# Kernel optimization log

Hardware: AMD Instinct MI355X
Metric: run time of the kernel (lower is better)

The kernel has to match this reference:

```python
import jax, jax.numpy as jnp
import numpy as np

NUM_HEADS = 14
NUM_KV_HEADS = 2
HEAD_DIM = 64
HIDDEN = 896
ROPE_THETA = 1000000.0
NEG_INF = -1e9


def _rope_tables(seq_len, dtype=jnp.float32):
    inv_freq = 1.0 / (ROPE_THETA ** (jnp.arange(0, HEAD_DIM, 2, dtype=jnp.float32) / HEAD_DIM))
    t = jnp.arange(seq_len, dtype=jnp.float32)
    freqs = t[:, None] * inv_freq[None, :]          # [S, hd/2]
    emb = jnp.concatenate((freqs, freqs), axis=-1)  # [S, hd]
    return jnp.cos(emb).astype(dtype), jnp.sin(emb).astype(dtype)


def _rotate_half(x):
    x1, x2 = x[..., : x.shape[-1] // 2], x[..., x.shape[-1] // 2 :]
    return jnp.concatenate((-x2, x1), axis=-1)


def setup_inputs() -> dict:
    key = jax.random.key(0)
    ks = jax.random.split(key, 6)
    B, S = 2, 2048
    hidden_states = jax.random.normal(ks[0], (B, S, HIDDEN), dtype=jnp.float32)
    # additive causal mask [1, 1, S, S]
    causal = jnp.tril(jnp.ones((S, S), dtype=bool))
    attention_mask = jnp.where(causal, 0.0, NEG_INF).astype(jnp.float32)[None, None]
    sd = 1.0 / np.sqrt(HIDDEN)
    Wq = jax.random.normal(ks[1], (HIDDEN, NUM_HEADS * HEAD_DIM), dtype=jnp.float32) * sd
    bq = jnp.zeros((NUM_HEADS * HEAD_DIM,), dtype=jnp.float32)
    Wk = jax.random.normal(ks[2], (HIDDEN, NUM_KV_HEADS * HEAD_DIM), dtype=jnp.float32) * sd
    bk = jnp.zeros((NUM_KV_HEADS * HEAD_DIM,), dtype=jnp.float32)
    Wv = jax.random.normal(ks[3], (HIDDEN, NUM_KV_HEADS * HEAD_DIM), dtype=jnp.float32) * sd
    bv = jnp.zeros((NUM_KV_HEADS * HEAD_DIM,), dtype=jnp.float32)
    Wo = jax.random.normal(ks[4], (NUM_HEADS * HEAD_DIM, HIDDEN), dtype=jnp.float32) * sd
    return {
        'hidden_states': hidden_states, 'attention_mask': attention_mask,
        'Wq': Wq, 'bq': bq, 'Wk': Wk, 'bk': bk, 'Wv': Wv, 'bv': bv, 'Wo': Wo,
    }


def reference(hidden_states, attention_mask, Wq, bq, Wk, bk, Wv, bv, Wo):
    B, S, _ = hidden_states.shape
    n_groups = NUM_HEADS // NUM_KV_HEADS
    q = (hidden_states @ Wq + bq).reshape(B, S, NUM_HEADS, HEAD_DIM)
    k = (hidden_states @ Wk + bk).reshape(B, S, NUM_KV_HEADS, HEAD_DIM)
    v = (hidden_states @ Wv + bv).reshape(B, S, NUM_KV_HEADS, HEAD_DIM)

    cos, sin = _rope_tables(S, hidden_states.dtype)
    cos = cos[None, :, None, :]
    sin = sin[None, :, None, :]
    q = q * cos + _rotate_half(q) * sin
    k = k * cos + _rotate_half(k) * sin

    # GQA: repeat kv heads to match query heads
    k = jnp.repeat(k, n_groups, axis=2)  # [B, S, nH, hd]
    v = jnp.repeat(v, n_groups, axis=2)

    q = q.transpose(0, 2, 1, 3)  # [B, nH, S, hd]
    k = k.transpose(0, 2, 1, 3)
    v = v.transpose(0, 2, 1, 3)

    scores = jnp.einsum('bhqd,bhkd->bhqk', q, k) / jnp.sqrt(jnp.float32(HEAD_DIM)).astype(q.dtype)
    scores = scores + attention_mask
    attn = jax.nn.softmax(scores, axis=-1)
    out = jnp.einsum('bhqk,bhkd->bhqd', attn, v)        # [B, nH, S, hd]
    out = out.transpose(0, 2, 1, 3).reshape(B, S, -1)   # [B, S, nH*hd]
    return out @ Wo
```

## Files before the change

### kernel.cpp

```cpp
#include <hip/hip_runtime.h>
#include <hip/hip_bf16.h>
#include <math.h>

#define NH 14
#define NKV 2
#define HD 64
#define HID 896
#define SEQ 2048
#define BATCH 2

typedef __attribute__((ext_vector_type(8))) short short8;
typedef __attribute__((ext_vector_type(4))) float f32x4;
typedef unsigned short ushort_t;

__device__ __forceinline__ unsigned short f2b(float f) {
    unsigned int u = __float_as_uint(f);
    unsigned int r = (u + 0x7fffu + ((u >> 16) & 1u)) >> 16;
    return (unsigned short)r;
}

__global__ __launch_bounds__(256) void xcast_kernel(
    const float* __restrict__ X, ushort_t* __restrict__ Xb)
{
    size_t i = ((size_t)blockIdx.x * 256 + threadIdx.x) * 8;
    float4 a = *(const float4*)(X + i);
    float4 b = *(const float4*)(X + i + 4);
    short8 o;
    o[0] = f2b(a.x); o[1] = f2b(a.y); o[2] = f2b(a.z); o[3] = f2b(a.w);
    o[4] = f2b(b.x); o[5] = f2b(b.y); o[6] = f2b(b.z); o[7] = f2b(b.w);
    *(short8*)(Xb + i) = o;
}

__global__ __launch_bounds__(256) void wtrans_kernel(
    const float* __restrict__ Wq, const float* __restrict__ Wk,
    const float* __restrict__ Wv, const float* __restrict__ Wo,
    ushort_t* __restrict__ WqkvT, ushort_t* __restrict__ WoT)
{
    __shared__ float tile[32][33];
    const int tx = threadIdx.x, ty = threadIdx.y;
    const int z = blockIdx.z;
    const float* src; ushort_t* dst; int N, rowoff;
    if      (z == 0) { src = Wq; dst = WqkvT; N = HID; rowoff = 0;    }
    else if (z == 1) { src = Wk; dst = WqkvT; N = 128; rowoff = 896;  }
    else if (z == 2) { src = Wv; dst = WqkvT; N = 128; rowoff = 1024; }
    else             { src = Wo; dst = WoT;   N = HID; rowoff = 0;    }
    const int k0 = blockIdx.x * 32;
    const int n0 = blockIdx.y * 32;
    if (n0 >= N) return;
    #pragma unroll
    for (int i = 0; i < 4; ++i)
        tile[ty * 4 + i][tx] = src[(size_t)(k0 + ty * 4 + i) * N + n0 + tx];
    __syncthreads();
    #pragma unroll
    for (int i = 0; i < 4; ++i)
        dst[(size_t)(rowoff + n0 + ty * 4 + i) * HID + k0 + tx]
            = f2b(tile[tx][ty * 4 + i]);
}

#define LDA 40
__global__ __launch_bounds__(256) void qkv_kernel(
    const ushort_t* __restrict__ Xb, const ushort_t* __restrict__ WqkvT,
    const float* __restrict__ bq, const float* __restrict__ bk,
    const float* __restrict__ bv,
    ushort_t* __restrict__ qbuf, ushort_t* __restrict__ kbuf,
    ushort_t* __restrict__ vbuf)
{
    __shared__ ushort_t Asb[128 * LDA];
    __shared__ ushort_t Bsb[64 * LDA];
    const int tid  = threadIdx.x;
    const int w    = tid >> 6;
    const int lane = tid & 63;
    const int quad = lane >> 4;
    const int l16  = lane & 15;
    const int m0 = blockIdx.x * 128;
    const int nt = blockIdx.y;
    const int nb = nt * 64;

    f32x4 acc[2][4];
    #pragma unroll
    for (int mf = 0; mf < 2; ++mf)
        #pragma unroll
        for (int nf = 0; nf < 4; ++nf) acc[mf][nf] = (f32x4){0.f, 0.f, 0.f, 0.f};

    for (int k0 = 0; k0 < HID; k0 += 32) {
        #pragma unroll
        for (int j = 0; j < 2; ++j) {
            int u = tid + j * 256;
            int row = u >> 2, c8 = u & 3;
            *(short8*)&Asb[row * LDA + c8 * 8] =
                *(const short8*)(Xb + (size_t)(m0 + row) * HID + k0 + c8 * 8);
        }
        {
            int row = tid >> 2, c8 = tid & 3;
            *(short8*)&Bsb[row * LDA + c8 * 8] =
                *(const short8*)(WqkvT + (size_t)(nb + row) * HID + k0 + c8 * 8);
        }
        __syncthreads();
        const ushort_t* Ab = &Asb[(w * 32 + l16) * LDA + quad * 8];
        short8 a0 = *(const short8*)Ab;
        short8 a1 = *(const short8*)(Ab + 16 * LDA);
        #pragma unroll
        for (int nf = 0; nf < 4; ++nf) {
            short8 bf = *(const short8*)&Bsb[(nf * 16 + l16) * LDA + quad * 8];
            acc[0][nf] = __builtin_amdgcn_mfma_f32_16x16x32_bf16(a0, bf, acc[0][nf], 0, 0, 0);
            acc[1][nf] = __builtin_amdgcn_mfma_f32_16x16x32_bf16(a1, bf, acc[1][nf], 0, 0, 0);
        }
        __syncthreads();
    }

    float bcol[4];
    #pragma unroll
    for (int f = 0; f < 4; ++f) {
        int d = f * 16 + l16;
        bcol[f] = (nt < 14) ? bq[nt * 64 + d]
                : (nt < 16) ? bk[(nt - 14) * 64 + d]
                            : bv[(nt - 16) * 64 + d];
    }
    const float lnth = 13.815510558f;
    float if0 = expf(-((float)l16)        / 32.0f * lnth);
    float if1 = expf(-((float)(l16 + 16)) / 32.0f * lnth);

    #pragma unroll
    for (int mf = 0; mf < 2; ++mf)
        #pragma unroll
        for (int r = 0; r < 4; ++r) {
            int grow = m0 + w * 32 + mf * 16 + quad * 4 + r;
            int b = grow >> 11;
            int s = grow & 2047;
            float v0 = acc[mf][0][r] + bcol[0];
            float v1 = acc[mf][1][r] + bcol[1];
            float v2 = acc[mf][2][r] + bcol[2];
            float v3 = acc[mf][3][r] + bcol[3];
            if (nt < 16) {
                float s0, c0, s1, c1;
                sincosf((float)s * if0, &s0, &c0);
                sincosf((float)s * if1, &s1, &c1);
                float n0 = v0 * c0 - v2 * s0;
                float n2 = v2 * c0 + v0 * s0;
                float n1 = v1 * c1 - v3 * s1;
                float n3 = v3 * c1 + v1 * s1;
                v0 = n0; v1 = n1; v2 = n2; v3 = n3;
            }
            if (nt < 14) {
                ushort_t* dst = qbuf + ((size_t)(b * NH + nt) * SEQ + s) * HD;
                dst[l16]      = f2b(v0);
                dst[l16 + 16] = f2b(v1);
                dst[l16 + 32] = f2b(v2);
                dst[l16 + 48] = f2b(v3);
            } else if (nt < 16) {
                ushort_t* dst = kbuf + ((size_t)(b * NKV + nt - 14) * SEQ + s) * HD;
                dst[l16]      = f2b(v0);
                dst[l16 + 16] = f2b(v1);
                dst[l16 + 32] = f2b(v2);
                dst[l16 + 48] = f2b(v3);
            } else {
                ushort_t* dst = vbuf + (size_t)(b * NKV + nt - 16) * HD * SEQ + s;
                dst[(size_t)(l16)      * SEQ] = f2b(v0);
                dst[(size_t)(l16 + 16) * SEQ] = f2b(v1);
                dst[(size_t)(l16 + 32) * SEQ] = f2b(v2);
                dst[(size_t)(l16 + 48) * SEQ] = f2b(v3);
            }
        }
}

#define LDP 72
__global__ __launch_bounds__(256) void attn_kernel(
    const ushort_t* __restrict__ qbuf, const ushort_t* __restrict__ kbuf,
    const ushort_t* __restrict__ vbuf, ushort_t* __restrict__ abuf)
{
    __shared__ ushort_t Ks[64 * LDP];
    __shared__ ushort_t Vt[64 * LDP];
    __shared__ ushort_t Ps[4][16 * LDP];

    const int tid  = threadIdx.x;
    const int w    = tid >> 6;
    const int lane = tid & 63;
    const int quad = lane >> 4;
    const int l16  = lane & 15;
    const int bi = blockIdx.x;
    const int h  = blockIdx.y;
    const int b  = blockIdx.z;
    const int kvh = h / (NH / NKV);

    const ushort_t* kb_h = kbuf + (size_t)(b * NKV + kvh) * SEQ * HD;
    const ushort_t* vt_h = vbuf + (size_t)(b * NKV + kvh) * HD * SEQ;

    for (int pass = 0; pass < 2; ++pass) {
        const int qt = pass ? (31 - bi) : bi;

        const ushort_t* qrow =
            qbuf + ((size_t)((b * NH + h) * SEQ) + qt * 64 + w * 16 + l16) * HD;
        short8 qf0 = *(const short8*)(qrow + quad * 8);
        short8 qf1 = *(const short8*)(qrow + 32 + quad * 8);

        f32x4 O[4];
        float m_i[4], l_i[4];
        #pragma unroll
        for (int n = 0; n < 4; ++n) O[n] = (f32x4){0.f, 0.f, 0.f, 0.f};
        #pragma unroll
        for (int r = 0; r < 4; ++r) { m_i[r] = -1e30f; l_i[r] = 0.0f; }

        for (int kt = 0; kt <= qt; ++kt) {
            __syncthreads();
            for (int i = tid; i < 512; i += 256) {
                int row = i >> 3, c8 = i & 7;
                *(short8*)&Ks[row * LDP + c8 * 8] =
                    *(const short8*)(kb_h + ((size_t)(kt * 64 + row)) * HD + c8 * 8);
                *(short8*)&Vt[row * LDP + c8 * 8] =
                    *(const short8*)(vt_h + (size_t)row * SEQ + kt * 64 + c8 * 8);
            }
            __syncthreads();

            f32x4 S[4];
            #pragma unroll
            for (int f = 0; f < 4; ++f) {
                S[f] = (f32x4){0.f, 0.f, 0.f, 0.f};
                short8 kf0 = *(const short8*)&Ks[(f * 16 + l16) * LDP + quad * 8];
                short8 kf1 = *(const short8*)&Ks[(f * 16 + l16) * LDP + 32 + quad * 8];
                S[f] = __builtin_amdgcn_mfma_f32_16x16x32_bf16(qf0, kf0, S[f], 0, 0, 0);
                S[f] = __builtin_amdgcn_mfma_f32_16x16x32_bf16(qf1, kf1, S[f], 0, 0, 0);
            }

            const bool diag = (kt == qt);
            float sc[4][4];
            #pragma unroll
            for (int f = 0; f < 4; ++f)
                #pragma unroll
                for (int r = 0; r < 4; ++r) {
                    float v = S[f][r] * 0.125f;
                    if (diag && (f * 16 + l16) > (w * 16 + quad * 4 + r)) v = -1e30f;
                    sc[f][r] = v;
                }

            float pm[4];
            #pragma unroll
            for (int r = 0; r < 4; ++r)
                pm[r] = fmaxf(fmaxf(sc[0][r], sc[1][r]), fmaxf(sc[2][r], sc[3][r]));
            #pragma unroll
            for (int off = 1; off < 16; off <<= 1)
                #pragma unroll
                for (int r = 0; r < 4; ++r)
                    pm[r] = fmaxf(pm[r], __shfl_xor(pm[r], off));

            float alpha[4], psum[4];
            #pragma unroll
            for (int r = 0; r < 4; ++r) {
                float mnew = fmaxf(m_i[r], pm[r]);
                alpha[r] = __expf(m_i[r] - mnew);
                m_i[r] = mnew;
                psum[r] = 0.0f;
            }
            #pragma unroll
            for (int f = 0; f < 4; ++f)
                #pragma unroll
                for (int r = 0; r < 4; ++r) {
                    float p = __expf(sc[f][r] - m_i[r]);
                    sc[f][r] = p;
                    psum[r] += p;
                }
            #pragma unroll
            for (int off = 1; off < 16; off <<= 1)
                #pragma unroll
                for (int r = 0; r < 4; ++r)
                    psum[r] += __shfl_xor(psum[r], off);
            #pragma unroll
            for (int r = 0; r < 4; ++r)
                l_i[r] = l_i[r] * alpha[r] + psum[r];
            #pragma unroll
            for (int n = 0; n < 4; ++n)
                #pragma unroll
                for (int r = 0; r < 4; ++r)
                    O[n][r] *= alpha[r];

            #pragma unroll
            for (int f = 0; f < 4; ++f)
                #pragma unroll
                for (int r = 0; r < 4; ++r)
                    Ps[w][(quad * 4 + r) * LDP + f * 16 + l16] = f2b(sc[f][r]);
            short8 pa0 = *(const short8*)&Ps[w][l16 * LDP + quad * 8];
            short8 pa1 = *(const short8*)&Ps[w][l16 * LDP + 32 + quad * 8];

            #pragma unroll
            for (int n = 0; n < 4; ++n) {
                short8 vf0 = *(const short8*)&Vt[(n * 16 + l16) * LDP + quad * 8];
                short8 vf1 = *(const short8*)&Vt[(n * 16 + l16) * LDP + 32 + quad * 8];
                O[n] = __builtin_amdgcn_mfma_f32_16x16x32_bf16(pa0, vf0, O[n], 0, 0, 0);
                O[n] = __builtin_amdgcn_mfma_f32_16x16x32_bf16(pa1, vf1, O[n], 0, 0, 0);
            }
        }

        float inv[4];
        #pragma unroll
        for (int r = 0; r < 4; ++r) inv[r] = 1.0f / l_i[r];
        #pragma unroll
        for (int n = 0; n < 4; ++n)
            #pragma unroll
            for (int r = 0; r < 4; ++r) {
                int rowg = qt * 64 + w * 16 + quad * 4 + r;
                abuf[(size_t)(b * SEQ + rowg) * HID + h * HD + n * 16 + l16]
                    = f2b(O[n][r] * inv[r]);
            }
    }
}

__global__ __launch_bounds__(256) void oproj_kernel(
    const ushort_t* __restrict__ A, const ushort_t* __restrict__ WoT,
    float* __restrict__ out)
{
    __shared__ ushort_t Asb[128 * LDA];
    __shared__ ushort_t Bsb[64 * LDA];
    const int tid  = threadIdx.x;
    const int w    = tid >> 6;
    const int lane = tid & 63;
    const int quad = lane >> 4;
    const int l16  = lane & 15;
    const int m0 = blockIdx.x * 128;
    const int n0 = blockIdx.y * 64;

    f32x4 acc[2][4];
    #pragma unroll
    for (int mf = 0; mf < 2; ++mf)
        #pragma unroll
        for (int nf = 0; nf < 4; ++nf) acc[mf][nf] = (f32x4){0.f, 0.f, 0.f, 0.f};

    for (int k0 = 0; k0 < HID; k0 += 32) {
        #pragma unroll
        for (int j = 0; j < 2; ++j) {
            int u = tid + j * 256;
            int row = u >> 2, c8 = u & 3;
            *(short8*)&Asb[row * LDA + c8 * 8] =
                *(const short8*)(A + (size_t)(m0 + row) * HID + k0 + c8 * 8);
        }
        {
            int row = tid >> 2, c8 = tid & 3;
            *(short8*)&Bsb[row * LDA + c8 * 8] =
                *(const short8*)(WoT + (size_t)(n0 + row) * HID + k0 + c8 * 8);
        }
        __syncthreads();
        const ushort_t* Ab = &Asb[(w * 32 + l16) * LDA + quad * 8];
        short8 a0 = *(const short8*)Ab;
        short8 a1 = *(const short8*)(Ab + 16 * LDA);
        #pragma unroll
        for (int nf = 0; nf < 4; ++nf) {
            short8 bf = *(const short8*)&Bsb[(nf * 16 + l16) * LDA + quad * 8];
            acc[0][nf] = __builtin_amdgcn_mfma_f32_16x16x32_bf16(a0, bf, acc[0][nf], 0, 0, 0);
            acc[1][nf] = __builtin_amdgcn_mfma_f32_16x16x32_bf16(a1, bf, acc[1][nf], 0, 0, 0);
        }
        __syncthreads();
    }

    #pragma unroll
    for (int mf = 0; mf < 2; ++mf)
        #pragma unroll
        for (int r = 0; r < 4; ++r) {
            size_t rbase = (size_t)(m0 + w * 32 + mf * 16 + quad * 4 + r) * HID + n0;
            #pragma unroll
            for (int f = 0; f < 4; ++f)
                out[rbase + f * 16 + l16] = acc[mf][f][r];
        }
}

extern "C" void kernel_launch(void* const* d_in, const int* in_sizes, int n_in,
                              void* d_out, int out_size, void* d_ws, size_t ws_size,
                              hipStream_t stream) {
    const float* X  = (const float*)d_in[0];
    const float* Wq = (const float*)d_in[2];
    const float* bq = (const float*)d_in[3];
    const float* Wk = (const float*)d_in[4];
    const float* bk = (const float*)d_in[5];
    const float* Wv = (const float*)d_in[6];
    const float* bv = (const float*)d_in[7];
    const float* Wo = (const float*)d_in[8];
    float* out = (float*)d_out;

    ushort_t* ws    = (ushort_t*)d_ws;
    ushort_t* Xb    = ws;
    ushort_t* WqkvT = Xb    + 3670016;
    ushort_t* WoT   = WqkvT + 1032192;
    ushort_t* qbuf  = WoT   + 802816;
    ushort_t* kbuf  = qbuf  + 3670016;
    ushort_t* vbuf  = kbuf  + 524288;
    ushort_t* abufb = vbuf  + 524288;

    xcast_kernel<<<dim3(1792), 256, 0, stream>>>(X, Xb);
    wtrans_kernel<<<dim3(28, 28, 4), dim3(32, 8), 0, stream>>>(
        Wq, Wk, Wv, Wo, WqkvT, WoT);
    qkv_kernel<<<dim3(32, 18), 256, 0, stream>>>(
        Xb, WqkvT, bq, bk, bv, qbuf, kbuf, vbuf);
    attn_kernel<<<dim3(16, NH, BATCH), 256, 0, stream>>>(
        qbuf, kbuf, vbuf, abufb);
    oproj_kernel<<<dim3(32, 14), 256, 0, stream>>>(
        abufb, WoT, out);
}
```

Baseline: 212.9 us.

## Restructure attention with transposed S, register-resident P, fp16 V and diagonal skipping

The attention kernel now computes S transposed (K as the A operand), so each lane owns one query row. This makes the softmax reductions two shuffles instead of four, and P can feed a 16x16x16 fp16 MFMA directly from registers, removing the shared-memory P round trip. V is stored as fp16, the 1/sqrt(d) scale is folded into Q in the projection kernel, and MFMAs on fully masked diagonal sub-tiles are skipped. The grid now launches one q-tile per block, longest first, instead of pairing tiles, which adds more blocks but risks load imbalance. The P and V products now run in fp16 instead of bf16.

```diff
diff --git a/kernel.cpp b/kernel.cpp
--- a/kernel.cpp
+++ b/kernel.cpp
@@ -10,7 +10,9 @@
 #define BATCH 2
 
 typedef __attribute__((ext_vector_type(8))) short short8;
+typedef __attribute__((ext_vector_type(4))) short short4v;
 typedef __attribute__((ext_vector_type(4))) float f32x4;
+typedef __attribute__((ext_vector_type(4))) _Float16 half4;
 typedef unsigned short ushort_t;
 
 __device__ __forceinline__ unsigned short f2b(float f) {
@@ -63,7 +65,7 @@
     const float* __restrict__ bq, const float* __restrict__ bk,
     const float* __restrict__ bv,
     ushort_t* __restrict__ qbuf, ushort_t* __restrict__ kbuf,
-    ushort_t* __restrict__ vbuf)
+    _Float16* __restrict__ vbuf)
 {
     __shared__ ushort_t Asb[128 * LDA];
     __shared__ ushort_t Bsb[64 * LDA];
@@ -143,10 +145,10 @@
             }
             if (nt < 14) {
                 ushort_t* dst = qbuf + ((size_t)(b * NH + nt) * SEQ + s) * HD;
-                dst[l16]      = f2b(v0);
-                dst[l16 + 16] = f2b(v1);
-                dst[l16 + 32] = f2b(v2);
-                dst[l16 + 48] = f2b(v3);
+                dst[l16]      = f2b(v0 * 0.125f);
+                dst[l16 + 16] = f2b(v1 * 0.125f);
+                dst[l16 + 32] = f2b(v2 * 0.125f);
+                dst[l16 + 48] = f2b(v3 * 0.125f);
             } else if (nt < 16) {
                 ushort_t* dst = kbuf + ((size_t)(b * NKV + nt - 14) * SEQ + s) * HD;
                 dst[l16]      = f2b(v0);
@@ -154,11 +156,11 @@
                 dst[l16 + 32] = f2b(v2);
                 dst[l16 + 48] = f2b(v3);
             } else {
-                ushort_t* dst = vbuf + (size_t)(b * NKV + nt - 16) * HD * SEQ + s;
-                dst[(size_t)(l16)      * SEQ] = f2b(v0);
-                dst[(size_t)(l16 + 16) * SEQ] = f2b(v1);
-                dst[(size_t)(l16 + 32) * SEQ] = f2b(v2);
-                dst[(size_t)(l16 + 48) * SEQ] = f2b(v3);
+                _Float16* dst = vbuf + (size_t)(b * NKV + nt - 16) * HD * SEQ + s;
+                dst[(size_t)(l16)      * SEQ] = (_Float16)v0;
+                dst[(size_t)(l16 + 16) * SEQ] = (_Float16)v1;
+                dst[(size_t)(l16 + 32) * SEQ] = (_Float16)v2;
+                dst[(size_t)(l16 + 48) * SEQ] = (_Float16)v3;
             }
         }
 }
@@ -166,140 +168,125 @@
 #define LDP 72
 __global__ __launch_bounds__(256) void attn_kernel(
     const ushort_t* __restrict__ qbuf, const ushort_t* __restrict__ kbuf,
-    const ushort_t* __restrict__ vbuf, ushort_t* __restrict__ abuf)
+    const _Float16* __restrict__ vbuf, ushort_t* __restrict__ abuf)
 {
     __shared__ ushort_t Ks[64 * LDP];
-    __shared__ ushort_t Vt[64 * LDP];
-    __shared__ ushort_t Ps[4][16 * LDP];
+    __shared__ _Float16 Vt[64 * LDP];
 
     const int tid  = threadIdx.x;
     const int w    = tid >> 6;
     const int lane = tid & 63;
     const int quad = lane >> 4;
     const int l16  = lane & 15;
-    const int bi = blockIdx.x;
+    const int qt = 31 - blockIdx.x;
     const int h  = blockIdx.y;
     const int b  = blockIdx.z;
     const int kvh = h / (NH / NKV);
+    const int myrow = w * 16 + l16;
 
     const ushort_t* kb_h = kbuf + (size_t)(b * NKV + kvh) * SEQ * HD;
-    const ushort_t* vt_h = vbuf + (size_t)(b * NKV + kvh) * HD * SEQ;
-
-    for (int pass = 0; pass < 2; ++pass) {
-        const int qt = pass ? (31 - bi) : bi;
-
-        const ushort_t* qrow =
-            qbuf + ((size_t)((b * NH + h) * SEQ) + qt * 64 + w * 16 + l16) * HD;
-        short8 qf0 = *(const short8*)(qrow + quad * 8);
-        short8 qf1 = *(const short8*)(qrow + 32 + quad * 8);
-
-        f32x4 O[4];
-        float m_i[4], l_i[4];
-        #pragma unroll
-        for (int n = 0; n < 4; ++n) O[n] = (f32x4){0.f, 0.f, 0.f, 0.f};
-        #pragma unroll
-        for (int r = 0; r < 4; ++r) { m_i[r] = -1e30f; l_i[r] = 0.0f; }
-
-        for (int kt = 0; kt <= qt; ++kt) {
-            __syncthreads();
-            for (int i = tid; i < 512; i += 256) {
-                int row = i >> 3, c8 = i & 7;
-                *(short8*)&Ks[row * LDP + c8 * 8] =
-                    *(const short8*)(kb_h + ((size_t)(kt * 64 + row)) * HD + c8 * 8);
-                *(short8*)&Vt[row * LDP + c8 * 8] =
-                    *(const short8*)(vt_h + (size_t)row * SEQ + kt * 64 + c8 * 8);
-            }
-            __syncthreads();
-
-            f32x4 S[4];
-            #pragma unroll
-            for (int f = 0; f < 4; ++f) {
-                S[f] = (f32x4){0.f, 0.f, 0.f, 0.f};
+    const _Float16* vt_h = vbuf + (size_t)(b * NKV + kvh) * HD * SEQ;
+
+    const ushort_t* qrow =
+        qbuf + ((size_t)((b * NH + h) * SEQ) + qt * 64 + myrow) * HD;
+    short8 qf0 = *(const short8*)(qrow + quad * 8);
+    short8 qf1 = *(const short8*)(qrow + 32 + quad * 8);
+
+    f32x4 O[4];
+    #pragma unroll
+    for (int mf = 0; mf < 4; ++mf) O[mf] = (f32x4){0.f, 0.f, 0.f, 0.f};
+    float m_i = -1e30f, l_i = 0.0f;
+
+    for (int kt = 0; kt <= qt; ++kt) {
+        __syncthreads();
+        for (int i = tid; i < 512; i += 256) {
+            int row = i >> 3, c8 = i & 7;
+            *(uint4*)&Ks[row * LDP + c8 * 8] =
+                *(const uint4*)(kb_h + ((size_t)(kt * 64 + row)) * HD + c8 * 8);
+            *(uint4*)&Vt[row * LDP + c8 * 8] =
+                *(const uint4*)(vt_h + (size_t)row * SEQ + kt * 64 + c8 * 8);
+        }
+        __syncthreads();
+
+        const bool diag = (kt == qt);
+
+        f32x4 S[4];
+        #pragma unroll
+        for (int f = 0; f < 4; ++f) {
+            S[f] = (f32x4){0.f, 0.f, 0.f, 0.f};
+            if (!diag || f <= w) {
                 short8 kf0 = *(const short8*)&Ks[(f * 16 + l16) * LDP + quad * 8];
                 short8 kf1 = *(const short8*)&Ks[(f * 16 + l16) * LDP + 32 + quad * 8];
-                S[f] = __builtin_amdgcn_mfma_f32_16x16x32_bf16(qf0, kf0, S[f], 0, 0, 0);
-                S[f] = __builtin_amdgcn_mfma_f32_16x16x32_bf16(qf1, kf1, S[f], 0, 0, 0);
-            }
-
-            const bool diag = (kt == qt);
-            float sc[4][4];
-            #pragma unroll
-            for (int f = 0; f < 4; ++f)
-                #pragma unroll
-                for (int r = 0; r < 4; ++r) {
-                    float v = S[f][r] * 0.125f;
-                    if (diag && (f * 16 + l16) > (w * 16 + quad * 4 + r)) v = -1e30f;
-                    sc[f][r] = v;
+                S[f] = __builtin_amdgcn_mfma_f32_16x16x32_bf16(kf0, qf0, S[f], 0, 0, 0);
+                S[f] = __builtin_amdgcn_mfma_f32_16x16x32_bf16(kf1, qf1, S[f], 0, 0, 0);
+            }
+        }
+
+        float sc[4][4];
+        float cmax = -1e30f;
+        #pragma unroll
+        for (int f = 0; f < 4; ++f)
+            #pragma unroll
+            for (int r = 0; r < 4; ++r) {
+                float v = S[f][r];
+                if (diag && (f * 16 + quad * 4 + r) > myrow) v = -1e30f;
+                sc[f][r] = v;
+                cmax = fmaxf(cmax, v);
+            }
+        cmax = fmaxf(cmax, __shfl_xor(cmax, 16));
+        cmax = fmaxf(cmax, __shfl_xor(cmax, 32));
+
+        float m_new = fmaxf(m_i, cmax);
+        float alpha = __expf(m_i - m_new);
+        m_i = m_new;
+
+        float psum = 0.0f;
+        #pragma unroll
+        for (int f = 0; f < 4; ++f)
+            #pragma unroll
+            for (int r = 0; r < 4; ++r) {
+                float p = __expf(sc[f][r] - m_new);
+                sc[f][r] = p;
+                psum += p;
+            }
+        psum += __shfl_xor(psum, 16);
+        psum += __shfl_xor(psum, 32);
+        l_i = l_i * alpha + psum;
+
+        #pragma unroll
+        for (int mf = 0; mf < 4; ++mf)
+            #pragma unroll
+            for (int r = 0; r < 4; ++r)
+                O[mf][r] *= alpha;
+
+        half4 pb[4];
+        #pragma unroll
+        for (int f = 0; f < 4; ++f)
+            #pragma unroll
+            for (int j = 0; j < 4; ++j)
+                pb[f][j] = (_Float16)sc[f][j];
+
+        #pragma unroll
+        for (int mf = 0; mf < 4; ++mf) {
+            const _Float16* vb = &Vt[(mf * 16 + l16) * LDP + quad * 4];
+            #pragma unroll
+            for (int kc = 0; kc < 4; ++kc) {
+                if (!diag || kc <= w) {
+                    half4 va = *(const half4*)(vb + kc * 16);
+                    O[mf] = __builtin_amdgcn_mfma_f32_16x16x16f16(va, pb[kc], O[mf], 0, 0, 0);
                 }
-
-            float pm[4];
-            #pragma unroll
-            for (int r = 0; r < 4; ++r)
-                pm[r] = fmaxf(fmaxf(sc[0][r], sc[1][r]), fmaxf(sc[2][r], sc[3][r]));
-            #pragma unroll
-            for (int off = 1; off < 16; off <<= 1)
-                #pragma unroll
-                for (int r = 0; r < 4; ++r)
-                    pm[r] = fmaxf(pm[r], __shfl_xor(pm[r], off));
-
-            float alpha[4], psum[4];
-            #pragma unroll
-            for (int r = 0; r < 4; ++r) {
-                float mnew = fmaxf(m_i[r], pm[r]);
-                alpha[r] = __expf(m_i[r] - mnew);
-                m_i[r] = mnew;
-                psum[r] = 0.0f;
-            }
-            #pragma unroll
-            for (int f = 0; f < 4; ++f)
-                #pragma unroll
-                for (int r = 0; r < 4; ++r) {
-                    float p = __expf(sc[f][r] - m_i[r]);
-                    sc[f][r] = p;
-                    psum[r] += p;
-                }
-            #pragma unroll
-            for (int off = 1; off < 16; off <<= 1)
-                #pragma unroll
-                for (int r = 0; r < 4; ++r)
-                    psum[r] += __shfl_xor(psum[r], off);
-            #pragma unroll
-            for (int r = 0; r < 4; ++r)
-                l_i[r] = l_i[r] * alpha[r] + psum[r];
-            #pragma unroll
-            for (int n = 0; n < 4; ++n)
-                #pragma unroll
-                for (int r = 0; r < 4; ++r)
-                    O[n][r] *= alpha[r];
-
-            #pragma unroll
-            for (int f = 0; f < 4; ++f)
-                #pragma unroll
-                for (int r = 0; r < 4; ++r)
-                    Ps[w][(quad * 4 + r) * LDP + f * 16 + l16] = f2b(sc[f][r]);
-            short8 pa0 = *(const short8*)&Ps[w][l16 * LDP + quad * 8];
-            short8 pa1 = *(const short8*)&Ps[w][l16 * LDP + 32 + quad * 8];
-
-            #pragma unroll
-            for (int n = 0; n < 4; ++n) {
-                short8 vf0 = *(const short8*)&Vt[(n * 16 + l16) * LDP + quad * 8];
-                short8 vf1 = *(const short8*)&Vt[(n * 16 + l16) * LDP + 32 + quad * 8];
-                O[n] = __builtin_amdgcn_mfma_f32_16x16x32_bf16(pa0, vf0, O[n], 0, 0, 0);
-                O[n] = __builtin_amdgcn_mfma_f32_16x16x32_bf16(pa1, vf1, O[n], 0, 0, 0);
-            }
-        }
-
-        float inv[4];
-        #pragma unroll
-        for (int r = 0; r < 4; ++r) inv[r] = 1.0f / l_i[r];
-        #pragma unroll
-        for (int n = 0; n < 4; ++n)
-            #pragma unroll
-            for (int r = 0; r < 4; ++r) {
-                int rowg = qt * 64 + w * 16 + quad * 4 + r;
-                abuf[(size_t)(b * SEQ + rowg) * HID + h * HD + n * 16 + l16]
-                    = f2b(O[n][r] * inv[r]);
-            }
+            }
+        }
+    }
+
+    float inv = 1.0f / l_i;
+    ushort_t* op = abuf + (size_t)(b * SEQ + qt * 64 + myrow) * HID + h * HD;
+    #pragma unroll
+    for (int mf = 0; mf < 4; ++mf) {
+        short4v st;
+        #pragma unroll
+        for (int r = 0; r < 4; ++r) st[r] = (short)f2b(O[mf][r] * inv);
+        *(short4v*)(op + mf * 16 + quad * 4) = st;
     }
 }
 
@@ -379,15 +366,15 @@
     ushort_t* WoT   = WqkvT + 1032192;
     ushort_t* qbuf  = WoT   + 802816;
     ushort_t* kbuf  = qbuf  + 3670016;
-    ushort_t* vbuf  = kbuf  + 524288;
-    ushort_t* abufb = vbuf  + 524288;
+    _Float16* vbuf  = (_Float16*)(kbuf + 524288);
+    ushort_t* abufb = (ushort_t*)vbuf + 524288;
 
     xcast_kernel<<<dim3(1792), 256, 0, stream>>>(X, Xb);
     wtrans_kernel<<<dim3(28, 28, 4), dim3(32, 8), 0, stream>>>(
         Wq, Wk, Wv, Wo, WqkvT, WoT);
     qkv_kernel<<<dim3(32, 18), 256, 0, stream>>>(
         Xb, WqkvT, bq, bk, bv, qbuf, kbuf, vbuf);
-    attn_kernel<<<dim3(16, NH, BATCH), 256, 0, stream>>>(
+    attn_kernel<<<dim3(32, NH, BATCH), 256, 0, stream>>>(
         qbuf, kbuf, vbuf, abufb);
     oproj_kernel<<<dim3(32, 14), 256, 0, stream>>>(
         abufb, WoT, out);
```

After: 220.0 us. 3.3% more time.

## Double-buffer LDS tiles with register prefetch in QKV and output projection GEMMs

Applied to the files above, without the earlier changes.

The QKV and output-projection GEMM loops now use two LDS buffers, with global loads prefetched into registers two steps ahead. This lets global memory latency overlap the MFMA work and drops one barrier per k-step. The attention kernel's LDS row pitch also changes from 72 to 76 to alter the bank mapping. The cost is doubled LDS use for the GEMM tiles and extra live registers.

```diff
diff --git a/kernel.cpp b/kernel.cpp
--- a/kernel.cpp
+++ b/kernel.cpp
@@ -8,6 +8,7 @@
 #define HID 896
 #define SEQ 2048
 #define BATCH 2
+#define KT 28
 
 typedef __attribute__((ext_vector_type(8))) short short8;
 typedef __attribute__((ext_vector_type(4))) float f32x4;
@@ -65,8 +66,8 @@
     ushort_t* __restrict__ qbuf, ushort_t* __restrict__ kbuf,
     ushort_t* __restrict__ vbuf)
 {
-    __shared__ ushort_t Asb[128 * LDA];
-    __shared__ ushort_t Bsb[64 * LDA];
+    __shared__ ushort_t Asb[2][128 * LDA];
+    __shared__ ushort_t Bsb[2][64 * LDA];
     const int tid  = threadIdx.x;
     const int w    = tid >> 6;
     const int lane = tid & 63;
@@ -76,36 +77,51 @@
     const int nt = blockIdx.y;
     const int nb = nt * 64;
 
+    const int ar0 = tid >> 2;
+    const int ac8 = tid & 3;
+    const ushort_t* Ag0 = Xb + (size_t)(m0 + ar0) * HID + ac8 * 8;
+    const ushort_t* Ag1 = Xb + (size_t)(m0 + ar0 + 64) * HID + ac8 * 8;
+    const ushort_t* Bg  = WqkvT + (size_t)(nb + ar0) * HID + ac8 * 8;
+
     f32x4 acc[2][4];
     #pragma unroll
     for (int mf = 0; mf < 2; ++mf)
         #pragma unroll
         for (int nf = 0; nf < 4; ++nf) acc[mf][nf] = (f32x4){0.f, 0.f, 0.f, 0.f};
 
-    for (int k0 = 0; k0 < HID; k0 += 32) {
-        #pragma unroll
-        for (int j = 0; j < 2; ++j) {
-            int u = tid + j * 256;
-            int row = u >> 2, c8 = u & 3;
-            *(short8*)&Asb[row * LDA + c8 * 8] =
-                *(const short8*)(Xb + (size_t)(m0 + row) * HID + k0 + c8 * 8);
-        }
-        {
-            int row = tid >> 2, c8 = tid & 3;
-            *(short8*)&Bsb[row * LDA + c8 * 8] =
-                *(const short8*)(WqkvT + (size_t)(nb + row) * HID + k0 + c8 * 8);
-        }
+    short8 aReg0, aReg1, bReg;
+    aReg0 = *(const short8*)(Ag0);
+    aReg1 = *(const short8*)(Ag1);
+    bReg  = *(const short8*)(Bg);
+    *(short8*)&Asb[0][ar0 * LDA + ac8 * 8]        = aReg0;
+    *(short8*)&Asb[0][(ar0 + 64) * LDA + ac8 * 8] = aReg1;
+    *(short8*)&Bsb[0][ar0 * LDA + ac8 * 8]        = bReg;
+    aReg0 = *(const short8*)(Ag0 + 32);
+    aReg1 = *(const short8*)(Ag1 + 32);
+    bReg  = *(const short8*)(Bg  + 32);
+
+    for (int ks = 0; ks < KT; ++ks) {
         __syncthreads();
-        const ushort_t* Ab = &Asb[(w * 32 + l16) * LDA + quad * 8];
+        const int cur = ks & 1;
+        if (ks + 1 < KT) {
+            *(short8*)&Asb[cur ^ 1][ar0 * LDA + ac8 * 8]        = aReg0;
+            *(short8*)&Asb[cur ^ 1][(ar0 + 64) * LDA + ac8 * 8] = aReg1;
+            *(short8*)&Bsb[cur ^ 1][ar0 * LDA + ac8 * 8]        = bReg;
+        }
+        if (ks + 2 < KT) {
+            aReg0 = *(const short8*)(Ag0 + (ks + 2) * 32);
+            aReg1 = *(const short8*)(Ag1 + (ks + 2) * 32);
+            bReg  = *(const short8*)(Bg  + (ks + 2) * 32);
+        }
+        const ushort_t* Ab = &Asb[cur][(w * 32 + l16) * LDA + quad * 8];
         short8 a0 = *(const short8*)Ab;
         short8 a1 = *(const short8*)(Ab + 16 * LDA);
         #pragma unroll
         for (int nf = 0; nf < 4; ++nf) {
-            short8 bf = *(const short8*)&Bsb[(nf * 16 + l16) * LDA + quad * 8];
+            short8 bf = *(const short8*)&Bsb[cur][(nf * 16 + l16) * LDA + quad * 8];
             acc[0][nf] = __builtin_amdgcn_mfma_f32_16x16x32_bf16(a0, bf, acc[0][nf], 0, 0, 0);
             acc[1][nf] = __builtin_amdgcn_mfma_f32_16x16x32_bf16(a1, bf, acc[1][nf], 0, 0, 0);
         }
-        __syncthreads();
     }
 
     float bcol[4];
@@ -163,7 +179,7 @@
         }
 }
 
-#define LDP 72
+#define LDP 76
 __global__ __launch_bounds__(256) void attn_kernel(
     const ushort_t* __restrict__ qbuf, const ushort_t* __restrict__ kbuf,
     const ushort_t* __restrict__ vbuf, ushort_t* __restrict__ abuf)
@@ -307,8 +323,8 @@
     const ushort_t* __restrict__ A, const ushort_t* __restrict__ WoT,
     float* __restrict__ out)
 {
-    __shared__ ushort_t Asb[128 * LDA];
-    __shared__ ushort_t Bsb[64 * LDA];
+    __shared__ ushort_t Asb[2][128 * LDA];
+    __shared__ ushort_t Bsb[2][64 * LDA];
     const int tid  = threadIdx.x;
     const int w    = tid >> 6;
     const int lane = tid & 63;
@@ -317,36 +333,51 @@
     const int m0 = blockIdx.x * 128;
     const int n0 = blockIdx.y * 64;
 
+    const int ar0 = tid >> 2;
+    const int ac8 = tid & 3;
+    const ushort_t* Ag0 = A + (size_t)(m0 + ar0) * HID + ac8 * 8;
+    const ushort_t* Ag1 = A + (size_t)(m0 + ar0 + 64) * HID + ac8 * 8;
+    const ushort_t* Bg  = WoT + (size_t)(n0 + ar0) * HID + ac8 * 8;
+
     f32x4 acc[2][4];
     #pragma unroll
     for (int mf = 0; mf < 2; ++mf)
         #pragma unroll
         for (int nf = 0; nf < 4; ++nf) acc[mf][nf] = (f32x4){0.f, 0.f, 0.f, 0.f};
 
-    for (int k0 = 0; k0 < HID; k0 += 32) {
-        #pragma unroll
-        for (int j = 0; j < 2; ++j) {
-            int u = tid + j * 256;
-            int row = u >> 2, c8 = u & 3;
-            *(short8*)&Asb[row * LDA + c8 * 8] =
-                *(const short8*)(A + (size_t)(m0 + row) * HID + k0 + c8 * 8);
-        }
-        {
-            int row = tid >> 2, c8 = tid & 3;
-            *(short8*)&Bsb[row * LDA + c8 * 8] =
-                *(const short8*)(WoT + (size_t)(n0 + row) * HID + k0 + c8 * 8);
-        }
+    short8 aReg0, aReg1, bReg;
+    aReg0 = *(const short8*)(Ag0);
+    aReg1 = *(const short8*)(Ag1);
+    bReg  = *(const short8*)(Bg);
+    *(short8*)&Asb[0][ar0 * LDA + ac8 * 8]        = aReg0;
+    *(short8*)&Asb[0][(ar0 + 64) * LDA + ac8 * 8] = aReg1;
+    *(short8*)&Bsb[0][ar0 * LDA + ac8 * 8]        = bReg;
+    aReg0 = *(const short8*)(Ag0 + 32);
+    aReg1 = *(const short8*)(Ag1 + 32);
+    bReg  = *(const short8*)(Bg  + 32);
+
+    for (int ks = 0; ks < KT; ++ks) {
         __syncthreads();
-        const ushort_t* Ab = &Asb[(w * 32 + l16) * LDA + quad * 8];
+        const int cur = ks & 1;
+        if (ks + 1 < KT) {
+            *(short8*)&Asb[cur ^ 1][ar0 * LDA + ac8 * 8]        = aReg0;
+            *(short8*)&Asb[cur ^ 1][(ar0 + 64) * LDA + ac8 * 8] = aReg1;
+            *(short8*)&Bsb[cur ^ 1][ar0 * LDA + ac8 * 8]        = bReg;
+        }
+        if (ks + 2 < KT) {
+            aReg0 = *(const short8*)(Ag0 + (ks + 2) * 32);
+            aReg1 = *(const short8*)(Ag1 + (ks + 2) * 32);
+            bReg  = *(const short8*)(Bg  + (ks + 2) * 32);
+        }
+        const ushort_t* Ab = &Asb[cur][(w * 32 + l16) * LDA + quad * 8];
         short8 a0 = *(const short8*)Ab;
         short8 a1 = *(const short8*)(Ab + 16 * LDA);
         #pragma unroll
         for (int nf = 0; nf < 4; ++nf) {
-            short8 bf = *(const short8*)&Bsb[(nf * 16 + l16) * LDA + quad * 8];
+            short8 bf = *(const short8*)&Bsb[cur][(nf * 16 + l16) * LDA + quad * 8];
             acc[0][nf] = __builtin_amdgcn_mfma_f32_16x16x32_bf16(a0, bf, acc[0][nf], 0, 0, 0);
             acc[1][nf] = __builtin_amdgcn_mfma_f32_16x16x32_bf16(a1, bf, acc[1][nf], 0, 0, 0);
         }
-        __syncthreads();
     }
 
     #pragma unroll
```

Measured after the change: 207.7 us. 1.02x faster.
